# Kernel tuning notes

Measured on AMD Instinct MI355X. Metric: run time of the kernel, lower is better.

## Reference

```python
import jax, jax.numpy as jnp
import numpy as np

N_NODES = 100000
N_EDGES = 1600000
IN_DIM = 64
HID = 128
N_CLASSES = 1
N_GRAPHS = 512


def _glorot(key, shape):
    fan_in, fan_out = shape[0], shape[1]
    lim = (6.0 / (fan_in + fan_out)) ** 0.5
    return jax.random.uniform(key, shape, jnp.float32, -lim, lim)


def setup_inputs() -> dict:
    key = jax.random.key(0)
    ks = jax.random.split(key, 10)
    x = jax.random.normal(ks[0], (N_NODES, IN_DIM), jnp.float32)
    edge_src = jax.random.randint(ks[1], (N_EDGES,), 0, N_NODES)
    edge_dst = jax.random.randint(ks[2], (N_EDGES,), 0, N_NODES)
    graph_ids = jnp.sort(jax.random.randint(ks[3], (N_NODES,), 0, N_GRAPHS))
    return {
        "x": x,
        "edge_src": edge_src,
        "edge_dst": edge_dst,
        "graph_ids": graph_ids,
        "W1": _glorot(ks[4], (IN_DIM, HID)),
        "b1": jnp.zeros((HID,), jnp.float32),
        "W2": _glorot(ks[5], (HID, HID)),
        "b2": jnp.zeros((HID,), jnp.float32),
        "Wc1": _glorot(ks[6], (HID, HID)),
        "bc1": jnp.zeros((HID,), jnp.float32),
        "Wc2": _glorot(ks[7], (HID, HID)),
        "bc2": jnp.zeros((HID,), jnp.float32),
        "Wc3": _glorot(ks[8], (HID, N_CLASSES)),
        "bc3": jnp.zeros((N_CLASSES,), jnp.float32),
    }


def _graph_conv(h, edge_src, edge_dst, W, b):
    # DGL GraphConv, norm='both': out = D_out^{-1/2} A D_in^{-1/2} h W + b
    ones = jnp.ones((edge_src.shape[0],), h.dtype)
    deg_out = jnp.clip(jax.ops.segment_sum(ones, edge_src, num_segments=N_NODES), 1.0)
    deg_in = jnp.clip(jax.ops.segment_sum(ones, edge_dst, num_segments=N_NODES), 1.0)
    h = h * jax.lax.rsqrt(deg_out)[:, None]           # src-side norm
    agg = jax.ops.segment_sum(h[edge_src], edge_dst, num_segments=N_NODES)  # [N, D]
    agg = agg * jax.lax.rsqrt(deg_in)[:, None]        # dst-side norm
    return agg @ W + b


def reference(x, edge_src, edge_dst, graph_ids, W1, b1, W2, b2, Wc1, bc1, Wc2, bc2, Wc3, bc3):
    h = jax.nn.relu(_graph_conv(x, edge_src, edge_dst, W1, b1))
    h = jax.nn.relu(_graph_conv(h, edge_src, edge_dst, W2, b2))
    # mean_nodes pooling over batched graphs
    sums = jax.ops.segment_sum(h, graph_ids, num_segments=N_GRAPHS)  # [G, H]
    cnts = jax.ops.segment_sum(jnp.ones((N_NODES,), h.dtype), graph_ids, num_segments=N_GRAPHS)
    hg = sums / jnp.clip(cnts, 1.0)[:, None]
    out = jax.nn.relu(hg @ Wc1 + bc1)
    out = jax.nn.relu(out @ Wc2 + bc2)
    return out @ Wc3 + bc3  # [G, n_classes]
```

## Files before the change

### kernel.cpp

```cpp
#include <hip/hip_runtime.h>

#define N_NODES 100000
#define N_EDGES 1600000
#define IN_DIM 64
#define HID 128
#define N_GRAPHS 512
#define NBUCK 391

__global__ __launch_bounds__(256) void k_bhist(const int* __restrict__ src, const int* __restrict__ dst,
                                               int* __restrict__ dcnt, int* __restrict__ scnt) {
    __shared__ int hd[NBUCK];
    __shared__ int hs[NBUCK];
    const int t = threadIdx.x;
    const int e0 = blockIdx.x * 4096 + t * 16;
    for (int i = t; i < NBUCK; i += 256) { hd[i] = 0; hs[i] = 0; }
    __syncthreads();
    if (e0 < N_EDGES) {
        const int4* d4 = (const int4*)(dst + e0);
        const int4* s4 = (const int4*)(src + e0);
#pragma unroll
        for (int u = 0; u < 4; ++u) {
            int4 d = d4[u], s = s4[u];
            atomicAdd(&hd[d.x >> 8], 1); atomicAdd(&hd[d.y >> 8], 1);
            atomicAdd(&hd[d.z >> 8], 1); atomicAdd(&hd[d.w >> 8], 1);
            atomicAdd(&hs[s.x >> 8], 1); atomicAdd(&hs[s.y >> 8], 1);
            atomicAdd(&hs[s.z >> 8], 1); atomicAdd(&hs[s.w >> 8], 1);
        }
    }
    __syncthreads();
    for (int i = t; i < NBUCK; i += 256) {
        if (hd[i]) atomicAdd(&dcnt[i], hd[i]);
        if (hs[i]) atomicAdd(&scnt[i], hs[i]);
    }
}

__global__ __launch_bounds__(512) void k_bscan3(const int* __restrict__ dcnt, const int* __restrict__ scnt,
                                                const int* __restrict__ gid,
                                                int* __restrict__ dbase, int* __restrict__ sbase,
                                                int* __restrict__ dcur, int* __restrict__ scur,
                                                int* __restrict__ gstart) {
    const int t = threadIdx.x;
    if (blockIdx.x == 2) {
        for (int g = t; g <= N_GRAPHS; g += 512) {
            int lo = 0, hi = N_NODES;
            while (lo < hi) {
                int mid = (lo + hi) >> 1;
                if (gid[mid] < g) lo = mid + 1; else hi = mid;
            }
            gstart[g] = lo;
        }
        return;
    }
    __shared__ int l[512];
    const int* cntp = (blockIdx.x == 0) ? dcnt : scnt;
    int* basep = (blockIdx.x == 0) ? dbase : sbase;
    int* curp  = (blockIdx.x == 0) ? dcur  : scur;
    int v = (t < NBUCK) ? cntp[t] : 0;
    l[t] = v;
    __syncthreads();
    for (int off = 1; off < 512; off <<= 1) {
        int x = (t >= off) ? l[t - off] : 0;
        __syncthreads();
        l[t] += x;
        __syncthreads();
    }
    if (t < NBUCK) {
        int excl = l[t] - v;
        basep[t] = excl; curp[t] = excl;
    }
    if (t == NBUCK - 1) basep[NBUCK] = l[t];
}

__global__ __launch_bounds__(256) void k_bin2(const int* __restrict__ src, const int* __restrict__ dst,
                                              int* __restrict__ dcur, int* __restrict__ scur,
                                              int* __restrict__ binnedD, int* __restrict__ binnedS) {
    __shared__ int hd[NBUCK];
    __shared__ int bd[NBUCK];
    __shared__ int hs[NBUCK];
    __shared__ int bs[NBUCK];
    const int t = threadIdx.x;
    const int e0 = blockIdx.x * 4096 + t * 16;
    for (int i = t; i < NBUCK; i += 256) { hd[i] = 0; hs[i] = 0; }
    __syncthreads();
    if (e0 < N_EDGES) {
        const int4* d4 = (const int4*)(dst + e0);
        const int4* s4 = (const int4*)(src + e0);
#pragma unroll
        for (int u = 0; u < 4; ++u) {
            int4 d = d4[u], s = s4[u];
            atomicAdd(&hd[d.x >> 8], 1); atomicAdd(&hd[d.y >> 8], 1);
            atomicAdd(&hd[d.z >> 8], 1); atomicAdd(&hd[d.w >> 8], 1);
            atomicAdd(&hs[s.x >> 8], 1); atomicAdd(&hs[s.y >> 8], 1);
            atomicAdd(&hs[s.z >> 8], 1); atomicAdd(&hs[s.w >> 8], 1);
        }
    }
    __syncthreads();
    for (int i = t; i < NBUCK; i += 256) {
        int c = hd[i];
        bd[i] = c ? atomicAdd(&dcur[i], c) : 0;
        hd[i] = 0;
        c = hs[i];
        bs[i] = c ? atomicAdd(&scur[i], c) : 0;
        hs[i] = 0;
    }
    __syncthreads();
    if (e0 < N_EDGES) {
        const int4* d4 = (const int4*)(dst + e0);
        const int4* s4 = (const int4*)(src + e0);
#pragma unroll
        for (int u = 0; u < 4; ++u) {
            int4 d = d4[u];
            int4 s = s4[u];
            int bk, r;
            bk = d.x >> 8; r = atomicAdd(&hd[bk], 1); binnedD[bd[bk] + r] = s.x | ((d.x & 255) << 17);
            bk = d.y >> 8; r = atomicAdd(&hd[bk], 1); binnedD[bd[bk] + r] = s.y | ((d.y & 255) << 17);
            bk = d.z >> 8; r = atomicAdd(&hd[bk], 1); binnedD[bd[bk] + r] = s.z | ((d.z & 255) << 17);
            bk = d.w >> 8; r = atomicAdd(&hd[bk], 1); binnedD[bd[bk] + r] = s.w | ((d.w & 255) << 17);
            bk = s.x >> 8; r = atomicAdd(&hs[bk], 1); binnedS[bs[bk] + r] = s.x;
            bk = s.y >> 8; r = atomicAdd(&hs[bk], 1); binnedS[bs[bk] + r] = s.y;
            bk = s.z >> 8; r = atomicAdd(&hs[bk], 1); binnedS[bs[bk] + r] = s.z;
            bk = s.w >> 8; r = atomicAdd(&hs[bk], 1); binnedS[bs[bk] + r] = s.w;
        }
    }
}

__global__ __launch_bounds__(256) void k_prep2(const int* __restrict__ dbase, const int* __restrict__ sbase,
                                               const int* __restrict__ binnedD, const int* __restrict__ binnedS,
                                               int* __restrict__ rowp, float* __restrict__ rsi,
                                               float* __restrict__ rso, int* __restrict__ col) {
    const int t = threadIdx.x;
    if (blockIdx.x < NBUCK) {
        const int b = blockIdx.x;
        const int n0 = b * 256;
        __shared__ int cnt[256];
        __shared__ int scn[256];
        __shared__ int cur[256];
        __shared__ int sb[2];
        if (t < 2) sb[t] = dbase[b + t];
        cnt[t] = 0;
        __syncthreads();
        const int s = sb[0], e = sb[1];
        for (int i = s + t; i < e; i += 256) atomicAdd(&cnt[binnedD[i] >> 17], 1);
        __syncthreads();
        const int c = cnt[t];
        scn[t] = c;
        __syncthreads();
        for (int off = 1; off < 256; off <<= 1) {
            int v = (t >= off) ? scn[t - off] : 0;
            __syncthreads();
            scn[t] += v;
            __syncthreads();
        }
        const int excl = scn[t] - c;
        cur[t] = excl;
        if (n0 + t < N_NODES) {
            rowp[n0 + t] = s + excl;
            rsi[n0 + t] = 1.0f / sqrtf(fmaxf((float)c, 1.0f));
        }
        if (b == NBUCK - 1 && t == 0) rowp[N_NODES] = e;
        __syncthreads();
        for (int i = s + t; i < e; i += 256) {
            int p = binnedD[i];
            int r = atomicAdd(&cur[p >> 17], 1);
            col[s + r] = p & 0x1FFFF;
        }
    } else {
        const int b = blockIdx.x - NBUCK;
        const int n0 = b * 256;
        __shared__ int cnt2[256];
        __shared__ int sb2[2];
        if (t < 2) sb2[t] = sbase[b + t];
        cnt2[t] = 0;
        __syncthreads();
        const int s = sb2[0], e = sb2[1];
        for (int i = s + t; i < e; i += 256) atomicAdd(&cnt2[binnedS[i] - n0], 1);
        __syncthreads();
        if (n0 + t < N_NODES) rso[n0 + t] = 1.0f / sqrtf(fmaxf((float)cnt2[t], 1.0f));
    }
}

__global__ __launch_bounds__(256) void k_gather64(const float4* __restrict__ x4, const float* __restrict__ rso,
                                                  const int* __restrict__ rowp, const int* __restrict__ col,
                                                  float4* __restrict__ agg4) {
    int wv = (blockIdx.x * 256 + threadIdx.x) >> 6;
    if (wv >= N_NODES) return;
    int lane = threadIdx.x & 63;
    int grp = lane >> 4, li = lane & 15;
    int s = rowp[wv], e = rowp[wv + 1];
    float ax = 0.f, ay = 0.f, az = 0.f, aw = 0.f;
    int i = s + grp;
    for (; i + 12 < e; i += 16) {
        int c0 = col[i], c1 = col[i + 4], c2 = col[i + 8], c3 = col[i + 12];
        float4 v0 = x4[c0 * 16 + li];
        float4 v1 = x4[c1 * 16 + li];
        float4 v2 = x4[c2 * 16 + li];
        float4 v3 = x4[c3 * 16 + li];
        float r0 = rso[c0], r1 = rso[c1], r2 = rso[c2], r3 = rso[c3];
        ax = fmaf(r0, v0.x, ax); ay = fmaf(r0, v0.y, ay); az = fmaf(r0, v0.z, az); aw = fmaf(r0, v0.w, aw);
        ax = fmaf(r1, v1.x, ax); ay = fmaf(r1, v1.y, ay); az = fmaf(r1, v1.z, az); aw = fmaf(r1, v1.w, aw);
        ax = fmaf(r2, v2.x, ax); ay = fmaf(r2, v2.y, ay); az = fmaf(r2, v2.z, az); aw = fmaf(r2, v2.w, aw);
        ax = fmaf(r3, v3.x, ax); ay = fmaf(r3, v3.y, ay); az = fmaf(r3, v3.z, az); aw = fmaf(r3, v3.w, aw);
    }
    for (; i + 4 < e; i += 8) {
        int c0 = col[i], c1 = col[i + 4];
        float4 v0 = x4[c0 * 16 + li];
        float4 v1 = x4[c1 * 16 + li];
        float r0 = rso[c0], r1 = rso[c1];
        ax = fmaf(r0, v0.x, ax); ay = fmaf(r0, v0.y, ay); az = fmaf(r0, v0.z, az); aw = fmaf(r0, v0.w, aw);
        ax = fmaf(r1, v1.x, ax); ay = fmaf(r1, v1.y, ay); az = fmaf(r1, v1.z, az); aw = fmaf(r1, v1.w, aw);
    }
    for (; i < e; i += 4) {
        int c = col[i];
        float4 v = x4[c * 16 + li];
        float r = rso[c];
        ax = fmaf(r, v.x, ax); ay = fmaf(r, v.y, ay); az = fmaf(r, v.z, az); aw = fmaf(r, v.w, aw);
    }
    ax += __shfl_xor(ax, 16, 64); ay += __shfl_xor(ay, 16, 64);
    az += __shfl_xor(az, 16, 64); aw += __shfl_xor(aw, 16, 64);
    ax += __shfl_xor(ax, 32, 64); ay += __shfl_xor(ay, 32, 64);
    az += __shfl_xor(az, 32, 64); aw += __shfl_xor(aw, 32, 64);
    if (lane < 16) {
        float4 o; o.x = ax; o.y = ay; o.z = az; o.w = aw;
        agg4[wv * 16 + li] = o;
    }
}

template <int K, bool SCALE_OUT>
__global__ __launch_bounds__(256) void k_mm(const float* __restrict__ A, const float* __restrict__ W,
                                            const float* __restrict__ bias, const float* __restrict__ rsi,
                                            const float* __restrict__ rso, float* __restrict__ out) {
    __shared__ float WL[32 * 128];
    __shared__ float aL[64][33];
    const int t = threadIdx.x;
    const int jq = t & 31;
    const int ns = t >> 5;
    const int n0 = blockIdx.x * 64;
    float acc[8][4] = {};
    for (int kc = 0; kc < K; kc += 32) {
        const float4* Wg = (const float4*)(W + kc * 128);
        float4* WL4 = (float4*)WL;
#pragma unroll
        for (int u = 0; u < 4; ++u) WL4[t + 256 * u] = Wg[t + 256 * u];
        {
            int r = t >> 2, q = t & 3;
            int node = n0 + r;
#pragma unroll
            for (int h = 0; h < 2; ++h) {
                int qq = q + h * 4;
                float4 v = make_float4(0.f, 0.f, 0.f, 0.f);
                if (node < N_NODES) v = *(const float4*)(A + (size_t)node * K + kc + qq * 4);
                aL[r][qq * 4 + 0] = v.x; aL[r][qq * 4 + 1] = v.y;
                aL[r][qq * 4 + 2] = v.z; aL[r][qq * 4 + 3] = v.w;
            }
        }
        __syncthreads();
#pragma unroll
        for (int k = 0; k < 32; ++k) {
            float4 wv = ((const float4*)WL)[k * 32 + jq];
#pragma unroll
            for (int i = 0; i < 8; ++i) {
                float av = aL[ns * 8 + i][k];
                acc[i][0] += av * wv.x; acc[i][1] += av * wv.y;
                acc[i][2] += av * wv.z; acc[i][3] += av * wv.w;
            }
        }
        __syncthreads();
    }
#pragma unroll
    for (int i = 0; i < 8; ++i) {
        int node = n0 + ns * 8 + i;
        if (node >= N_NODES) continue;
        float ri = rsi[node];
        float ro = SCALE_OUT ? rso[node] : 1.0f;
        float4 bj = ((const float4*)bias)[jq];
        float4 o;
        o.x = fmaxf(acc[i][0] * ri + bj.x, 0.f) * ro;
        o.y = fmaxf(acc[i][1] * ri + bj.y, 0.f) * ro;
        o.z = fmaxf(acc[i][2] * ri + bj.z, 0.f) * ro;
        o.w = fmaxf(acc[i][3] * ri + bj.w, 0.f) * ro;
        *(float4*)(out + node * HID + jq * 4) = o;
    }
}

__global__ __launch_bounds__(256, 4) void k_g128p(const float4* __restrict__ h4, const int* __restrict__ rowp,
                                                  const int* __restrict__ col, const float* __restrict__ W,
                                                  const float* __restrict__ bias, const float* __restrict__ rsi,
                                                  const int* __restrict__ gid, float* __restrict__ gsum) {
    __shared__ float agg[32][HID];
    __shared__ float WL[32 * 128];
    __shared__ float gpart[8][128];
    const int t = threadIdx.x;
    const int wid = t >> 6, lane = t & 63;
    const int n0 = blockIdx.x * 32;
    for (int u = t; u < 8 * 128; u += 256) ((float*)gpart)[u] = 0.f;

    const int grp = lane >> 5, li = lane & 31;
#pragma unroll 1
    for (int it = 0; it < 8; ++it) {
        const int node = n0 + wid * 8 + it;
        const int s = rowp[node], e = rowp[node + 1];
        float ax = 0.f, ay = 0.f, az = 0.f, aw = 0.f;
        int i = s + grp;
        for (; i + 6 < e; i += 8) {
            int c0 = col[i], c1 = col[i + 2], c2 = col[i + 4], c3 = col[i + 6];
            float4 v0 = h4[c0 * 32 + li];
            float4 v1 = h4[c1 * 32 + li];
            float4 v2 = h4[c2 * 32 + li];
            float4 v3 = h4[c3 * 32 + li];
            ax += v0.x + v1.x + v2.x + v3.x;
            ay += v0.y + v1.y + v2.y + v3.y;
            az += v0.z + v1.z + v2.z + v3.z;
            aw += v0.w + v1.w + v2.w + v3.w;
        }
        for (; i < e; i += 2) {
            float4 v = h4[col[i] * 32 + li];
            ax += v.x; ay += v.y; az += v.z; aw += v.w;
        }
        ax += __shfl_xor(ax, 32, 64); ay += __shfl_xor(ay, 32, 64);
        az += __shfl_xor(az, 32, 64); aw += __shfl_xor(aw, 32, 64);
        if (lane < 32) {
            float4 o; o.x = ax; o.y = ay; o.z = az; o.w = aw;
            ((float4*)agg[node - n0])[li] = o;
        }
    }
    __syncthreads();

    const int jq = t & 31;
    const int ns = t >> 5;
    float acc[4][4] = {};
    for (int kc = 0; kc < HID; kc += 32) {
        const float4* Wg = (const float4*)(W + kc * 128);
        float4* WL4 = (float4*)WL;
#pragma unroll
        for (int u = 0; u < 4; ++u) WL4[t + 256 * u] = Wg[t + 256 * u];
        __syncthreads();
#pragma unroll
        for (int k = 0; k < 32; ++k) {
            float4 wv = ((const float4*)WL)[k * 32 + jq];
#pragma unroll
            for (int i = 0; i < 4; ++i) {
                float av = agg[ns * 4 + i][kc + k];
                acc[i][0] += av * wv.x; acc[i][1] += av * wv.y;
                acc[i][2] += av * wv.z; acc[i][3] += av * wv.w;
            }
        }
        __syncthreads();
    }

    const int g0 = gid[n0];
    float4 bj = ((const float4*)bias)[jq];
    int curslot = -9;
    float p0 = 0.f, p1 = 0.f, p2 = 0.f, p3 = 0.f;
#pragma unroll
    for (int i = 0; i < 4; ++i) {
        int node = n0 + ns * 4 + i;
        float ri = rsi[node];
        float ox = fmaxf(acc[i][0] * ri + bj.x, 0.f);
        float oy = fmaxf(acc[i][1] * ri + bj.y, 0.f);
        float oz = fmaxf(acc[i][2] * ri + bj.z, 0.f);
        float ow = fmaxf(acc[i][3] * ri + bj.w, 0.f);
        int slot = gid[node] - g0;
        if (slot != curslot) {
            if (curslot >= 0) {
                if (curslot < 8) {
                    atomicAdd(&gpart[curslot][jq * 4 + 0], p0);
                    atomicAdd(&gpart[curslot][jq * 4 + 1], p1);
                    atomicAdd(&gpart[curslot][jq * 4 + 2], p2);
                    atomicAdd(&gpart[curslot][jq * 4 + 3], p3);
                } else {
                    atomicAdd(&gsum[(g0 + curslot) * HID + jq * 4 + 0], p0);
                    atomicAdd(&gsum[(g0 + curslot) * HID + jq * 4 + 1], p1);
                    atomicAdd(&gsum[(g0 + curslot) * HID + jq * 4 + 2], p2);
                    atomicAdd(&gsum[(g0 + curslot) * HID + jq * 4 + 3], p3);
                }
            }
            curslot = slot; p0 = ox; p1 = oy; p2 = oz; p3 = ow;
        } else {
            p0 += ox; p1 += oy; p2 += oz; p3 += ow;
        }
    }
    if (curslot >= 0) {
        if (curslot < 8) {
            atomicAdd(&gpart[curslot][jq * 4 + 0], p0);
            atomicAdd(&gpart[curslot][jq * 4 + 1], p1);
            atomicAdd(&gpart[curslot][jq * 4 + 2], p2);
            atomicAdd(&gpart[curslot][jq * 4 + 3], p3);
        } else {
            atomicAdd(&gsum[(g0 + curslot) * HID + jq * 4 + 0], p0);
            atomicAdd(&gsum[(g0 + curslot) * HID + jq * 4 + 1], p1);
            atomicAdd(&gsum[(g0 + curslot) * HID + jq * 4 + 2], p2);
            atomicAdd(&gsum[(g0 + curslot) * HID + jq * 4 + 3], p3);
        }
    }
    __syncthreads();
    for (int u = t; u < 8 * 128; u += 256) {
        int slot = u >> 7, c = u & 127;
        float v = gpart[slot][c];
        if (v != 0.f) {
            int g = g0 + slot;
            if (g < N_GRAPHS) atomicAdd(&gsum[g * HID + c], v);
        }
    }
}

__global__ __launch_bounds__(128) void k_head(const float* __restrict__ gsum, const int* __restrict__ gstart,
                                              const float* __restrict__ Wc1, const float* __restrict__ bc1,
                                              const float* __restrict__ Wc2, const float* __restrict__ bc2,
                                              const float* __restrict__ Wc3, const float* __restrict__ bc3,
                                              float* __restrict__ out) {
    int g = blockIdx.x, t = threadIdx.x;
    int s = gstart[g], e = gstart[g + 1];
    float cnt = fmaxf((float)(e - s), 1.0f);
    __shared__ float buf[HID];
    __shared__ float red[2];
    buf[t] = gsum[g * HID + t] / cnt;
    __syncthreads();
    float a = bc1[t];
#pragma unroll 8
    for (int k = 0; k < HID; ++k) a += buf[k] * Wc1[k * HID + t];
    a = fmaxf(a, 0.f);
    __syncthreads();
    buf[t] = a;
    __syncthreads();
    float b = bc2[t];
#pragma unroll 8
    for (int k = 0; k < HID; ++k) b += buf[k] * Wc2[k * HID + t];
    b = fmaxf(b, 0.f);
    float p = b * Wc3[t];
    for (int off = 32; off > 0; off >>= 1) p += __shfl_down(p, off, 64);
    if ((t & 63) == 0) red[t >> 6] = p;
    __syncthreads();
    if (t == 0) out[g] = red[0] + red[1] + bc3[0];
}

extern "C" void kernel_launch(void* const* d_in, const int* in_sizes, int n_in,
                              void* d_out, int out_size, void* d_ws, size_t ws_size,
                              hipStream_t stream) {
    const float* x   = (const float*)d_in[0];
    const int* esrc  = (const int*)d_in[1];
    const int* edst  = (const int*)d_in[2];
    const int* gid   = (const int*)d_in[3];
    const float* W1  = (const float*)d_in[4];
    const float* b1  = (const float*)d_in[5];
    const float* W2  = (const float*)d_in[6];
    const float* b2  = (const float*)d_in[7];
    const float* Wc1 = (const float*)d_in[8];
    const float* bc1 = (const float*)d_in[9];
    const float* Wc2 = (const float*)d_in[10];
    const float* bc2 = (const float*)d_in[11];
    const float* Wc3 = (const float*)d_in[12];
    const float* bc3 = (const float*)d_in[13];
    float* out = (float*)d_out;

    char* w = (char*)d_ws;
    size_t off = 0;
    auto alloc = [&](size_t bytes) -> char* {
        char* p = w + off;
        off += (bytes + 255) & ~(size_t)255;
        return p;
    };
    int* dcnt   = (int*)alloc((size_t)2 * (NBUCK + 1) * 4);
    int* scnt   = dcnt + (NBUCK + 1);
    int* dbase  = (int*)alloc((size_t)(NBUCK + 1) * 4);
    int* sbase  = (int*)alloc((size_t)(NBUCK + 1) * 4);
    int* dcur   = (int*)alloc((size_t)NBUCK * 4);
    int* scur   = (int*)alloc((size_t)NBUCK * 4);
    float* rso  = (float*)alloc((size_t)N_NODES * 4);
    float* rsi  = (float*)alloc((size_t)N_NODES * 4);
    int* rowp   = (int*)alloc((size_t)(N_NODES + 1) * 4);
    int* gstart = (int*)alloc((size_t)(N_GRAPHS + 1) * 4);
    int* col    = (int*)alloc((size_t)N_EDGES * 4);
    float* gsum = (float*)alloc((size_t)N_GRAPHS * HID * 4);
    float* R1   = (float*)alloc((size_t)N_NODES * HID * 4);
    float* R2   = (float*)alloc((size_t)N_NODES * HID * 4);
    int* binnedD = (int*)R1;
    int* binnedS = (int*)R1 + (size_t)N_EDGES;
    float* agg1 = R1;
    float* h1s  = R2;

    (void)in_sizes; (void)n_in; (void)out_size; (void)ws_size;

    hipMemsetAsync(dcnt, 0, (size_t)2 * (NBUCK + 1) * 4, stream);
    hipMemsetAsync(gsum, 0, (size_t)N_GRAPHS * HID * 4, stream);

    const int BB = (N_EDGES + 4095) / 4096;
    const int GB = (N_NODES * 64 + 255) / 256;
    const int MB64 = (N_NODES + 63) / 64;
    const int FB32 = N_NODES / 32;

    k_bhist<<<BB, 256, 0, stream>>>(esrc, edst, dcnt, scnt);
    k_bscan3<<<3, 512, 0, stream>>>(dcnt, scnt, gid, dbase, sbase, dcur, scur, gstart);
    k_bin2<<<BB, 256, 0, stream>>>(esrc, edst, dcur, scur, binnedD, binnedS);
    k_prep2<<<2 * NBUCK, 256, 0, stream>>>(dbase, sbase, binnedD, binnedS, rowp, rsi, rso, col);
    k_gather64<<<GB, 256, 0, stream>>>((const float4*)x, rso, rowp, col, (float4*)agg1);
    k_mm<IN_DIM, true><<<MB64, 256, 0, stream>>>(agg1, W1, b1, rsi, rso, h1s);
    k_g128p<<<FB32, 256, 0, stream>>>((const float4*)h1s, rowp, col, W2, b2, rsi, gid, gsum);
    k_head<<<N_GRAPHS, 128, 0, stream>>>(gsum, gstart, Wc1, bc1, Wc2, bc2, Wc3, bc3, out);
}
```

Measured before the change: 338.6 us.

## Fuse layer-1 gather with its matmul and read weights directly from global

Layer-1 neighbour aggregation and the 64x128 matmul now run in one kernel. The aggregated rows stay in shared memory instead of being written to and re-read from a global buffer, which removes one kernel launch and that round trip. Both fused kernels also drop the shared-memory staging of W and its barriers, reading W as float4 straight from global/L2. Occupancy hints are raised to 8 blocks per CU. The risk is that W is now re-read from cache by every block, and the tighter register budget may cause spills.

```diff
diff --git a/kernel.cpp b/kernel.cpp
--- a/kernel.cpp
+++ b/kernel.cpp
@@ -179,115 +179,93 @@
     }
 }
 
-__global__ __launch_bounds__(256) void k_gather64(const float4* __restrict__ x4, const float* __restrict__ rso,
+__global__ __launch_bounds__(256, 8) void k_g64mm(const float4* __restrict__ x4, const float* __restrict__ rso,
                                                   const int* __restrict__ rowp, const int* __restrict__ col,
-                                                  float4* __restrict__ agg4) {
-    int wv = (blockIdx.x * 256 + threadIdx.x) >> 6;
-    if (wv >= N_NODES) return;
-    int lane = threadIdx.x & 63;
-    int grp = lane >> 4, li = lane & 15;
-    int s = rowp[wv], e = rowp[wv + 1];
-    float ax = 0.f, ay = 0.f, az = 0.f, aw = 0.f;
-    int i = s + grp;
-    for (; i + 12 < e; i += 16) {
-        int c0 = col[i], c1 = col[i + 4], c2 = col[i + 8], c3 = col[i + 12];
-        float4 v0 = x4[c0 * 16 + li];
-        float4 v1 = x4[c1 * 16 + li];
-        float4 v2 = x4[c2 * 16 + li];
-        float4 v3 = x4[c3 * 16 + li];
-        float r0 = rso[c0], r1 = rso[c1], r2 = rso[c2], r3 = rso[c3];
-        ax = fmaf(r0, v0.x, ax); ay = fmaf(r0, v0.y, ay); az = fmaf(r0, v0.z, az); aw = fmaf(r0, v0.w, aw);
-        ax = fmaf(r1, v1.x, ax); ay = fmaf(r1, v1.y, ay); az = fmaf(r1, v1.z, az); aw = fmaf(r1, v1.w, aw);
-        ax = fmaf(r2, v2.x, ax); ay = fmaf(r2, v2.y, ay); az = fmaf(r2, v2.z, az); aw = fmaf(r2, v2.w, aw);
-        ax = fmaf(r3, v3.x, ax); ay = fmaf(r3, v3.y, ay); az = fmaf(r3, v3.z, az); aw = fmaf(r3, v3.w, aw);
-    }
-    for (; i + 4 < e; i += 8) {
-        int c0 = col[i], c1 = col[i + 4];
-        float4 v0 = x4[c0 * 16 + li];
-        float4 v1 = x4[c1 * 16 + li];
-        float r0 = rso[c0], r1 = rso[c1];
-        ax = fmaf(r0, v0.x, ax); ay = fmaf(r0, v0.y, ay); az = fmaf(r0, v0.z, az); aw = fmaf(r0, v0.w, aw);
-        ax = fmaf(r1, v1.x, ax); ay = fmaf(r1, v1.y, ay); az = fmaf(r1, v1.z, az); aw = fmaf(r1, v1.w, aw);
-    }
-    for (; i < e; i += 4) {
-        int c = col[i];
-        float4 v = x4[c * 16 + li];
-        float r = rso[c];
-        ax = fmaf(r, v.x, ax); ay = fmaf(r, v.y, ay); az = fmaf(r, v.z, az); aw = fmaf(r, v.w, aw);
-    }
-    ax += __shfl_xor(ax, 16, 64); ay += __shfl_xor(ay, 16, 64);
-    az += __shfl_xor(az, 16, 64); aw += __shfl_xor(aw, 16, 64);
-    ax += __shfl_xor(ax, 32, 64); ay += __shfl_xor(ay, 32, 64);
-    az += __shfl_xor(az, 32, 64); aw += __shfl_xor(aw, 32, 64);
-    if (lane < 16) {
-        float4 o; o.x = ax; o.y = ay; o.z = az; o.w = aw;
-        agg4[wv * 16 + li] = o;
-    }
-}
-
-template <int K, bool SCALE_OUT>
-__global__ __launch_bounds__(256) void k_mm(const float* __restrict__ A, const float* __restrict__ W,
-                                            const float* __restrict__ bias, const float* __restrict__ rsi,
-                                            const float* __restrict__ rso, float* __restrict__ out) {
-    __shared__ float WL[32 * 128];
-    __shared__ float aL[64][33];
-    const int t = threadIdx.x;
+                                                  const float* __restrict__ W, const float* __restrict__ bias,
+                                                  const float* __restrict__ rsi, float* __restrict__ out) {
+    __shared__ float aggL[32][IN_DIM];
+    const int t = threadIdx.x;
+    const int wid = t >> 6, lane = t & 63;
+    const int n0 = blockIdx.x * 32;
+
+    const int grp = lane >> 4, li = lane & 15;
+#pragma unroll 1
+    for (int it = 0; it < 8; ++it) {
+        const int node = n0 + wid * 8 + it;
+        const int s = rowp[node], e = rowp[node + 1];
+        float ax = 0.f, ay = 0.f, az = 0.f, aw = 0.f;
+        int i = s + grp;
+        for (; i + 12 < e; i += 16) {
+            int c0 = col[i], c1 = col[i + 4], c2 = col[i + 8], c3 = col[i + 12];
+            float4 v0 = x4[c0 * 16 + li];
+            float4 v1 = x4[c1 * 16 + li];
+            float4 v2 = x4[c2 * 16 + li];
+            float4 v3 = x4[c3 * 16 + li];
+            float r0 = rso[c0], r1 = rso[c1], r2 = rso[c2], r3 = rso[c3];
+            ax = fmaf(r0, v0.x, ax); ay = fmaf(r0, v0.y, ay); az = fmaf(r0, v0.z, az); aw = fmaf(r0, v0.w, aw);
+            ax = fmaf(r1, v1.x, ax); ay = fmaf(r1, v1.y, ay); az = fmaf(r1, v1.z, az); aw = fmaf(r1, v1.w, aw);
+            ax = fmaf(r2, v2.x, ax); ay = fmaf(r2, v2.y, ay); az = fmaf(r2, v2.z, az); aw = fmaf(r2, v2.w, aw);
+            ax = fmaf(r3, v3.x, ax); ay = fmaf(r3, v3.y, ay); az = fmaf(r3, v3.z, az); aw = fmaf(r3, v3.w, aw);
+        }
+        for (; i + 4 < e; i += 8) {
+            int c0 = col[i], c1 = col[i + 4];
+            float4 v0 = x4[c0 * 16 + li];
+            float4 v1 = x4[c1 * 16 + li];
+            float r0 = rso[c0], r1 = rso[c1];
+            ax = fmaf(r0, v0.x, ax); ay = fmaf(r0, v0.y, ay); az = fmaf(r0, v0.z, az); aw = fmaf(r0, v0.w, aw);
+            ax = fmaf(r1, v1.x, ax); ay = fmaf(r1, v1.y, ay); az = fmaf(r1, v1.z, az); aw = fmaf(r1, v1.w, aw);
+        }
+        for (; i < e; i += 4) {
+            int c = col[i];
+            float4 v = x4[c * 16 + li];
+            float r = rso[c];
+            ax = fmaf(r, v.x, ax); ay = fmaf(r, v.y, ay); az = fmaf(r, v.z, az); aw = fmaf(r, v.w, aw);
+        }
+        ax += __shfl_xor(ax, 16, 64); ay += __shfl_xor(ay, 16, 64);
+        az += __shfl_xor(az, 16, 64); aw += __shfl_xor(aw, 16, 64);
+        ax += __shfl_xor(ax, 32, 64); ay += __shfl_xor(ay, 32, 64);
+        az += __shfl_xor(az, 32, 64); aw += __shfl_xor(aw, 32, 64);
+        if (lane < 16) {
+            float4 o; o.x = ax; o.y = ay; o.z = az; o.w = aw;
+            ((float4*)aggL[node - n0])[li] = o;
+        }
+    }
+    __syncthreads();
+
     const int jq = t & 31;
     const int ns = t >> 5;
-    const int n0 = blockIdx.x * 64;
-    float acc[8][4] = {};
-    for (int kc = 0; kc < K; kc += 32) {
-        const float4* Wg = (const float4*)(W + kc * 128);
-        float4* WL4 = (float4*)WL;
-#pragma unroll
-        for (int u = 0; u < 4; ++u) WL4[t + 256 * u] = Wg[t + 256 * u];
-        {
-            int r = t >> 2, q = t & 3;
-            int node = n0 + r;
-#pragma unroll
-            for (int h = 0; h < 2; ++h) {
-                int qq = q + h * 4;
-                float4 v = make_float4(0.f, 0.f, 0.f, 0.f);
-                if (node < N_NODES) v = *(const float4*)(A + (size_t)node * K + kc + qq * 4);
-                aL[r][qq * 4 + 0] = v.x; aL[r][qq * 4 + 1] = v.y;
-                aL[r][qq * 4 + 2] = v.z; aL[r][qq * 4 + 3] = v.w;
-            }
-        }
-        __syncthreads();
-#pragma unroll
-        for (int k = 0; k < 32; ++k) {
-            float4 wv = ((const float4*)WL)[k * 32 + jq];
-#pragma unroll
-            for (int i = 0; i < 8; ++i) {
-                float av = aL[ns * 8 + i][k];
-                acc[i][0] += av * wv.x; acc[i][1] += av * wv.y;
-                acc[i][2] += av * wv.z; acc[i][3] += av * wv.w;
-            }
-        }
-        __syncthreads();
-    }
-#pragma unroll
-    for (int i = 0; i < 8; ++i) {
-        int node = n0 + ns * 8 + i;
-        if (node >= N_NODES) continue;
+    const float4* Wg = (const float4*)W;
+    float acc[4][4] = {};
+#pragma unroll 8
+    for (int k = 0; k < IN_DIM; ++k) {
+        float4 wv = Wg[k * 32 + jq];
+#pragma unroll
+        for (int i = 0; i < 4; ++i) {
+            float av = aggL[ns * 4 + i][k];
+            acc[i][0] += av * wv.x; acc[i][1] += av * wv.y;
+            acc[i][2] += av * wv.z; acc[i][3] += av * wv.w;
+        }
+    }
+    float4 bj = ((const float4*)bias)[jq];
+#pragma unroll
+    for (int i = 0; i < 4; ++i) {
+        int node = n0 + ns * 4 + i;
         float ri = rsi[node];
-        float ro = SCALE_OUT ? rso[node] : 1.0f;
-        float4 bj = ((const float4*)bias)[jq];
+        float ro = rso[node];
         float4 o;
         o.x = fmaxf(acc[i][0] * ri + bj.x, 0.f) * ro;
         o.y = fmaxf(acc[i][1] * ri + bj.y, 0.f) * ro;
         o.z = fmaxf(acc[i][2] * ri + bj.z, 0.f) * ro;
         o.w = fmaxf(acc[i][3] * ri + bj.w, 0.f) * ro;
-        *(float4*)(out + node * HID + jq * 4) = o;
-    }
-}
-
-__global__ __launch_bounds__(256, 4) void k_g128p(const float4* __restrict__ h4, const int* __restrict__ rowp,
+        *(float4*)(out + (size_t)node * HID + jq * 4) = o;
+    }
+}
+
+__global__ __launch_bounds__(256, 8) void k_g128p(const float4* __restrict__ h4, const int* __restrict__ rowp,
                                                   const int* __restrict__ col, const float* __restrict__ W,
                                                   const float* __restrict__ bias, const float* __restrict__ rsi,
                                                   const int* __restrict__ gid, float* __restrict__ gsum) {
     __shared__ float agg[32][HID];
-    __shared__ float WL[32 * 128];
     __shared__ float gpart[8][128];
     const int t = threadIdx.x;
     const int wid = t >> 6, lane = t & 63;
@@ -327,24 +305,17 @@
 
     const int jq = t & 31;
     const int ns = t >> 5;
+    const float4* Wg = (const float4*)W;
     float acc[4][4] = {};
-    for (int kc = 0; kc < HID; kc += 32) {
-        const float4* Wg = (const float4*)(W + kc * 128);
-        float4* WL4 = (float4*)WL;
-#pragma unroll
-        for (int u = 0; u < 4; ++u) WL4[t + 256 * u] = Wg[t + 256 * u];
-        __syncthreads();
-#pragma unroll
-        for (int k = 0; k < 32; ++k) {
-            float4 wv = ((const float4*)WL)[k * 32 + jq];
-#pragma unroll
-            for (int i = 0; i < 4; ++i) {
-                float av = agg[ns * 4 + i][kc + k];
-                acc[i][0] += av * wv.x; acc[i][1] += av * wv.y;
-                acc[i][2] += av * wv.z; acc[i][3] += av * wv.w;
-            }
-        }
-        __syncthreads();
+#pragma unroll 8
+    for (int k = 0; k < HID; ++k) {
+        float4 wv = Wg[k * 32 + jq];
+#pragma unroll
+        for (int i = 0; i < 4; ++i) {
+            float av = agg[ns * 4 + i][k];
+            acc[i][0] += av * wv.x; acc[i][1] += av * wv.y;
+            acc[i][2] += av * wv.z; acc[i][3] += av * wv.w;
+        }
     }
 
     const int g0 = gid[n0];
@@ -475,7 +446,6 @@
     float* R2   = (float*)alloc((size_t)N_NODES * HID * 4);
     int* binnedD = (int*)R1;
     int* binnedS = (int*)R1 + (size_t)N_EDGES;
-    float* agg1 = R1;
     float* h1s  = R2;
 
     (void)in_sizes; (void)n_in; (void)out_size; (void)ws_size;
@@ -484,16 +454,13 @@
     hipMemsetAsync(gsum, 0, (size_t)N_GRAPHS * HID * 4, stream);
 
     const int BB = (N_EDGES + 4095) / 4096;
-    const int GB = (N_NODES * 64 + 255) / 256;
-    const int MB64 = (N_NODES + 63) / 64;
     const int FB32 = N_NODES / 32;
 
     k_bhist<<<BB, 256, 0, stream>>>(esrc, edst, dcnt, scnt);
     k_bscan3<<<3, 512, 0, stream>>>(dcnt, scnt, gid, dbase, sbase, dcur, scur, gstart);
     k_bin2<<<BB, 256, 0, stream>>>(esrc, edst, dcur, scur, binnedD, binnedS);
     k_prep2<<<2 * NBUCK, 256, 0, stream>>>(dbase, sbase, binnedD, binnedS, rowp, rsi, rso, col);
-    k_gather64<<<GB, 256, 0, stream>>>((const float4*)x, rso, rowp, col, (float4*)agg1);
-    k_mm<IN_DIM, true><<<MB64, 256, 0, stream>>>(agg1, W1, b1, rsi, rso, h1s);
+    k_g64mm<<<FB32, 256, 0, stream>>>((const float4*)x, rso, rowp, col, W1, b1, rsi, h1s);
     k_g128p<<<FB32, 256, 0, stream>>>((const float4*)h1s, rowp, col, W2, b2, rsi, gid, gsum);
     k_head<<<N_GRAPHS, 128, 0, stream>>>(gsum, gstart, Wc1, bc1, Wc2, bc2, Wc3, bc3, out);
 }
```

New measurement: 354.4 us. 4.7% more time.
